# Kernel tuning notes

Measured on AMD Instinct MI355X. Metric: run time of the kernel, lower is better.

Reference implementation:

```python
import jax, jax.numpy as jnp
import numpy as np

NQ = 4  # n_qubits_per_head


def _apply_ry(state, theta, q):
    # state: (N, 2,2,2,2) real amplitudes; theta: (N,) per-element angle; wire q
    st = jnp.moveaxis(state, 1 + q, -1)
    c = jnp.cos(0.5 * theta).reshape(-1, 1, 1, 1)
    s = jnp.sin(0.5 * theta).reshape(-1, 1, 1, 1)
    a0, a1 = st[..., 0], st[..., 1]
    st = jnp.stack([c * a0 - s * a1, s * a0 + c * a1], axis=-1)
    return jnp.moveaxis(st, -1, 1 + q)


def _apply_cnot(state, ctrl, tgt):
    st = jnp.moveaxis(state, (1 + ctrl, 1 + tgt), (-2, -1))
    st = jnp.stack([st[..., 0, :], st[..., 1, ::-1]], axis=-2)
    return jnp.moveaxis(st, (-2, -1), (1 + ctrl, 1 + tgt))


def _quantum_circuit(x_in, par):
    # x_in: (N, NQ) data angles; par: (N, L, NQ) variational angles (per head, tiled)
    N = x_in.shape[0]
    L = par.shape[1]
    state = jnp.zeros((N, 2, 2, 2, 2), x_in.dtype).at[:, 0, 0, 0, 0].set(1.0)
    for l in range(L):
        for q in range(NQ):
            state = _apply_ry(state, par[:, l, q], q)
        for q in range(NQ - 1):
            state = _apply_cnot(state, q, q + 1)
        state = _apply_cnot(state, NQ - 1, 0)
    for q in range(NQ):
        state = _apply_ry(state, x_in[:, q], q)
    p = state * state  # probabilities (real amplitudes: only RY/CNOT gates)
    zs = []
    for q in range(NQ):
        st = jnp.moveaxis(p, 1 + q, -1)
        zs.append(jnp.sum(st[..., 0], axis=(1, 2, 3)) - jnp.sum(st[..., 1], axis=(1, 2, 3)))
    return jnp.stack(zs, axis=-1)  # (N, NQ)


def setup_inputs() -> dict:
    key = jax.random.key(0)
    ks = jax.random.split(key, 6)
    B, T, E, H, L = 4, 2048, 1024, 16, 2
    scale = 1.0 / np.sqrt(E)
    x = jax.random.normal(ks[0], (B, T, E), dtype=jnp.float32)
    Wq = jax.random.normal(ks[1], (E, E), dtype=jnp.float32) * scale
    Wk = jax.random.normal(ks[2], (E, E), dtype=jnp.float32) * scale
    Wv = jax.random.normal(ks[3], (E, E), dtype=jnp.float32) * scale
    Wo = jax.random.normal(ks[4], (E, E), dtype=jnp.float32) * scale
    qparams = jax.random.normal(ks[5], (H, L, NQ), dtype=jnp.float32)
    return {"x": x, "Wq": Wq, "Wk": Wk, "Wv": Wv, "Wo": Wo, "qparams": qparams}


def reference(x, Wq, Wk, Wv, Wo, qparams):
    B, T, E = x.shape
    H, L, _ = qparams.shape
    hd = E // H
    q = x @ Wq.T
    k = x @ Wk.T
    v = x @ Wv.T
    # NOTE: original scales by sqrt(embed_dim), not sqrt(head_dim)
    scores = jnp.einsum('bte,bse->bts', q, k) / jnp.sqrt(jnp.asarray(E, x.dtype))
    w = jax.nn.softmax(scores, axis=-1)
    out = jnp.einsum('bts,bse->bte', w, v)
    oh = out.reshape(B, T, H, hd)
    N = B * T * H
    xin = oh[..., :NQ].reshape(N, NQ)
    par = jnp.broadcast_to(qparams[None, None], (B, T, H, L, NQ)).reshape(N, L, NQ)
    z = _quantum_circuit(xin, par)  # (N, NQ)
    zfull = jnp.concatenate([z, jnp.zeros((N, hd - NQ), x.dtype)], axis=-1)
    return zfull.reshape(B, T, E) @ Wo.T
```

## Files before the change

kernel.cpp:

```cpp
#include <hip/hip_runtime.h>
#include <hip/hip_fp16.h>

typedef _Float16 half_t;
typedef __attribute__((ext_vector_type(8))) _Float16 half8;
typedef __attribute__((ext_vector_type(4))) float floatx4;

__device__ __forceinline__ void async_copy16(const void* src, void* dst_lds) {
  __builtin_amdgcn_global_load_lds(
      (__attribute__((address_space(1))) void*)src,
      (__attribute__((address_space(3))) void*)dst_lds, 16, 0, 0);
}

template<int BN, int EPI>
__global__ __launch_bounds__(256) void gemm_nt(
    const half_t* __restrict__ A, const half_t* __restrict__ B,
    void* __restrict__ Cout,
    int lda, int ldb, int ldc, int kIters, int zShift,
    long sAz1, long sBz1, long sCz1,
    long sAz2, long sBz2, long sCz2, float scale,
    const float* __restrict__ qab)
{
  constexpr int BM = 128;
  constexpr int WN = BN / 2;
  constexpr int AN = WN / 16;
  constexpr int RA = BM * 8 / 256;
  constexpr int RB = BN * 8 / 256;
  __shared__ __align__(16) half_t lA[BM * 64];
  __shared__ __align__(16) half_t lB[BN * 64];

  const int tid  = threadIdx.x;
  const int wave = tid >> 6, lane = tid & 63;
  const int wm = wave >> 1, wn = wave & 1;
  const int er = lane >> 4, ec = lane & 15;
  const int sw = ec & 7;

  const long z = blockIdx.z;
  const long z2 = z >> zShift;
  const long z1 = z - (z2 << zShift);
  const half_t* Ab = A + (long)blockIdx.x * BM * lda + z1 * sAz1 + z2 * sAz2;
  const half_t* Bb = B + (long)blockIdx.y * BN * ldb + z1 * sBz1 + z2 * sBz2;
  const long cz = z1 * sCz1 + z2 * sCz2;

  floatx4 acc[4][AN];
  #pragma unroll
  for (int i = 0; i < 4; i++)
    #pragma unroll
    for (int j = 0; j < AN; j++)
      acc[i][j] = (floatx4){0.f, 0.f, 0.f, 0.f};

  for (int ks = 0; ks < kIters; ++ks) {
    const half_t* Ak = Ab + ks * 64;
    const half_t* Bk = Bb + ks * 64;
    #pragma unroll
    for (int r = 0; r < RA; r++) {
      int s = r * 256 + tid;
      int row = s >> 3;
      int kq = (s & 7) ^ (row & 7);
      async_copy16(Ak + (long)row * lda + kq * 8,
                   &lA[(r * 256 + wave * 64) * 8]);
    }
    #pragma unroll
    for (int r = 0; r < RB; r++) {
      int s = r * 256 + tid;
      int row = s >> 3;
      int kq = (s & 7) ^ (row & 7);
      async_copy16(Bk + (long)row * ldb + kq * 8,
                   &lB[(r * 256 + wave * 64) * 8]);
    }
    __syncthreads();

    #pragma unroll
    for (int h = 0; h < 2; h++) {
      half8 af[4], bfv[AN];
      #pragma unroll
      for (int i = 0; i < 4; i++) {
        int row = wm * 64 + i * 16 + ec;
        af[i] = *(const half8*)&lA[row * 64 + (((h * 4 + er) ^ sw) * 8)];
      }
      #pragma unroll
      for (int j = 0; j < AN; j++) {
        int row = wn * WN + j * 16 + ec;
        bfv[j] = *(const half8*)&lB[row * 64 + (((h * 4 + er) ^ sw) * 8)];
      }
      #pragma unroll
      for (int i = 0; i < 4; i++)
        #pragma unroll
        for (int j = 0; j < AN; j++)
          acc[i][j] = __builtin_amdgcn_mfma_f32_16x16x32_f16(
              af[i], bfv[j], acc[i][j], 0, 0, 0);
    }
    __syncthreads();
  }

  const long rowBase = (long)blockIdx.x * BM + wm * 64;
  const long colBase = (long)blockIdx.y * BN + wn * WN;
  #pragma unroll
  for (int i = 0; i < 4; i++)
    #pragma unroll
    for (int j = 0; j < AN; j++)
      #pragma unroll
      for (int r = 0; r < 4; r++) {
        long row = rowBase + i * 16 + er * 4 + r;
        long col = colBase + j * 16 + ec;
        float v = acc[i][j][r];
        if constexpr (EPI == 0) {
          ((half_t*)Cout)[cz + row * (long)ldc + col] = (_Float16)(v * scale);
        } else if constexpr (EPI == 1) {
          ((half_t*)Cout)[cz + col * (long)ldc + row] = (_Float16)v;
        } else if constexpr (EPI == 2) {
          ((float*)Cout)[cz + row * (long)ldc + col] = v * scale;
        } else {
          float za = qab[2 * (int)col], zb = qab[2 * (int)col + 1];
          float zv = za * cosf(v) + zb * sinf(v);
          ((half_t*)Cout)[cz + row * (long)ldc + col] = (_Float16)zv;
        }
      }
}

__global__ __launch_bounds__(256) void softmax_rows(half_t* __restrict__ S,
                                                    int ld)
{
  const long row = blockIdx.x;
  half8* sp = (half8*)(S + row * (long)ld);
  const int t = threadIdx.x;
  const int wave = t >> 6, lane = t & 63;
  half8 hv = sp[t];
  float e[8];
  #pragma unroll
  for (int k = 0; k < 8; k++) e[k] = (float)hv[k];
  float m = e[0];
  #pragma unroll
  for (int k = 1; k < 8; k++) m = fmaxf(m, e[k]);
  #pragma unroll
  for (int o = 32; o > 0; o >>= 1) m = fmaxf(m, __shfl_xor(m, o));
  __shared__ float rmax[4], rsum[4];
  if (lane == 0) rmax[wave] = m;
  __syncthreads();
  m = fmaxf(fmaxf(rmax[0], rmax[1]), fmaxf(rmax[2], rmax[3]));
  float s = 0.f;
  #pragma unroll
  for (int k = 0; k < 8; k++) { e[k] = expf(e[k] - m); s += e[k]; }
  #pragma unroll
  for (int o = 32; o > 0; o >>= 1) s += __shfl_xor(s, o);
  if (lane == 0) rsum[wave] = s;
  __syncthreads();
  float inv = 1.f / (rsum[0] + rsum[1] + rsum[2] + rsum[3]);
  half8 o8;
  #pragma unroll
  for (int k = 0; k < 8; k++) o8[k] = (_Float16)(e[k] * inv);
  sp[t] = o8;
}

__global__ __launch_bounds__(256) void prep_all(
    const float* __restrict__ x,  const float* __restrict__ Wq,
    const float* __restrict__ Wk, const float* __restrict__ Wv,
    const float* __restrict__ Wo, const float* __restrict__ qp, int L,
    half_t* __restrict__ xh, half_t* __restrict__ Wqk,
    half_t* __restrict__ Wv4, half_t* __restrict__ Wos,
    float* __restrict__ qab)
{
  const int bid = blockIdx.x;
  if (bid < 4096) {
    long i = ((long)bid * 256 + threadIdx.x) * 8;
    float4 a = *(const float4*)(x + i);
    float4 b = *(const float4*)(x + i + 4);
    half8 h = {(_Float16)a.x, (_Float16)a.y, (_Float16)a.z, (_Float16)a.w,
               (_Float16)b.x, (_Float16)b.y, (_Float16)b.z, (_Float16)b.w};
    *(half8*)(xh + i) = h;
  } else if (bid < 5120) {
    long i = ((long)(bid - 4096) * 256 + threadIdx.x) * 8;
    int r = (int)(i >> 10);
    int e = (int)(i & 1023);
    const float* src = (r < 1024 ? Wq + (long)r * 1024
                                 : Wk + (long)(r - 1024) * 1024) + e;
    float4 a = *(const float4*)src;
    float4 b = *(const float4*)(src + 4);
    half8 h = {(_Float16)a.x, (_Float16)a.y, (_Float16)a.z, (_Float16)a.w,
               (_Float16)b.x, (_Float16)b.y, (_Float16)b.z, (_Float16)b.w};
    *(half8*)(Wqk + i) = h;
  } else if (bid < 5152) {
    long i = ((long)(bid - 5120) * 256 + threadIdx.x) * 8;
    int c = (int)(i >> 10);
    int e = (int)(i & 1023);
    const float* src = Wv + (long)(((c >> 2) << 6) | (c & 3)) * 1024 + e;
    float4 a = *(const float4*)src;
    float4 b = *(const float4*)(src + 4);
    half8 h = {(_Float16)a.x, (_Float16)a.y, (_Float16)a.z, (_Float16)a.w,
               (_Float16)b.x, (_Float16)b.y, (_Float16)b.z, (_Float16)b.w};
    *(half8*)(Wv4 + i) = h;
  } else if (bid < 5408) {
    int idx = (bid - 5152) * 256 + threadIdx.x;
    int e = idx >> 6, c = idx & 63;
    Wos[idx] = (_Float16)Wo[(long)e * 1024 + (((c >> 2) << 6) | (c & 3))];
  } else {
    int h = threadIdx.x;
    if (h >= 16) return;
    float st[16];
    #pragma unroll
    for (int i = 0; i < 16; i++) st[i] = 0.f;
    st[0] = 1.f;
    for (int l = 0; l < L; l++) {
      #pragma unroll
      for (int q = 0; q < 4; q++) {
        float th = qp[(h * L + l) * 4 + q];
        float c = cosf(0.5f * th), s = sinf(0.5f * th);
        int mq = 8 >> q;
        #pragma unroll
        for (int i = 0; i < 16; i++) {
          if ((i & mq) == 0) {
            float a0 = st[i], a1 = st[i | mq];
            st[i]      = c * a0 - s * a1;
            st[i | mq] = s * a0 + c * a1;
          }
        }
      }
      const int cm[4] = {8, 4, 2, 1};
      const int tm[4] = {4, 2, 1, 8};
      #pragma unroll
      for (int p = 0; p < 4; p++) {
        int mc = cm[p], mt = tm[p];
        #pragma unroll
        for (int i = 0; i < 16; i++) {
          if ((i & mc) != 0 && (i & mt) == 0) {
            float tv = st[i]; st[i] = st[i | mt]; st[i | mt] = tv;
          }
        }
      }
    }
    #pragma unroll
    for (int q = 0; q < 4; q++) {
      int mq = 8 >> q;
      float zc = 0.f, xc = 0.f;
      #pragma unroll
      for (int i = 0; i < 16; i++) {
        float p2 = st[i] * st[i];
        zc += ((i & mq) == 0) ? p2 : -p2;
        if ((i & mq) == 0) xc += st[i] * st[i | mq];
      }
      qab[(h * 4 + q) * 2 + 0] = zc;
      qab[(h * 4 + q) * 2 + 1] = -2.f * xc;
    }
  }
}

extern "C" void kernel_launch(void* const* d_in, const int* in_sizes, int n_in,
                              void* d_out, int out_size, void* d_ws, size_t ws_size,
                              hipStream_t stream)
{
  const float* x  = (const float*)d_in[0];
  const float* Wq = (const float*)d_in[1];
  const float* Wk = (const float*)d_in[2];
  const float* Wv = (const float*)d_in[3];
  const float* Wo = (const float*)d_in[4];
  const float* qp = (const float*)d_in[5];
  const int L = in_sizes[5] / 64;
  float* out = (float*)d_out;

  char* w = (char*)d_ws;
  size_t off = 0;
  auto alloc = [&](size_t bytes) -> void* {
    void* p = w + off;
    off = (off + bytes + 255) & ~(size_t)255;
    return p;
  };
  float*  qab  = (float*)alloc(512);
  half_t* xh   = (half_t*)alloc((size_t)8192 * 1024 * 2);
  half_t* Wqk  = (half_t*)alloc((size_t)2048 * 1024 * 2);
  half_t* Wv4  = (half_t*)alloc((size_t)64 * 1024 * 2);
  half_t* Wos  = (half_t*)alloc((size_t)1024 * 64 * 2);
  half_t* V4th = (half_t*)alloc((size_t)64 * 8192 * 2);
  half_t* Z4   = (half_t*)alloc((size_t)8192 * 64 * 2);

  half_t* QKb = (half_t*)d_out;

  int tier = (ws_size >= off + (size_t)8192 * 2048 * 2 + 256) ? 0 : 1;
  const size_t Sn = (tier == 0) ? (size_t)8192 * 2048 : (size_t)2048 * 2048;
  half_t* S = (half_t*)alloc(Sn * 2);

  prep_all<<<dim3(5409), dim3(256), 0, stream>>>(
      x, Wq, Wk, Wv, Wo, qp, L, xh, Wqk, Wv4, Wos, qab);

  gemm_nt<128, 0><<<dim3(64, 16, 1), 256, 0, stream>>>(
      xh, Wqk, QKb, 1024, 1024, 2048, 16, 0,
      0, 0, 0, 0, 0, 0, 1.f, nullptr);
  gemm_nt<64, 1><<<dim3(64, 1, 1), 256, 0, stream>>>(
      xh, Wv4, V4th, 1024, 1024, 8192, 16, 0,
      0, 0, 0, 0, 0, 0, 1.f, nullptr);

  if (tier == 0) {
    gemm_nt<128, 0><<<dim3(16, 16, 4), 256, 0, stream>>>(
        QKb, QKb + 1024, S, 2048, 2048, 2048, 16, 0,
        0, 0, 0, (long)2048 * 2048, (long)2048 * 2048, (long)2048 * 2048,
        0.03125f, nullptr);
    softmax_rows<<<dim3(8192), dim3(256), 0, stream>>>(S, 2048);
    gemm_nt<64, 5><<<dim3(16, 1, 4), 256, 0, stream>>>(
        S, V4th, Z4, 2048, 8192, 64, 32, 0,
        0, 0, 0, (long)2048 * 2048, 2048, (long)2048 * 64, 1.f, qab);
  } else {
    for (int b = 0; b < 4; b++) {
      const long q0 = (long)b * 2048;
      gemm_nt<128, 0><<<dim3(16, 16, 1), 256, 0, stream>>>(
          QKb + q0 * 2048, QKb + 1024 + q0 * 2048, S,
          2048, 2048, 2048, 16, 0, 0, 0, 0, 0, 0, 0, 0.03125f, nullptr);
      softmax_rows<<<dim3(2048), dim3(256), 0, stream>>>(S, 2048);
      gemm_nt<64, 5><<<dim3(16, 1, 1), 256, 0, stream>>>(
          S, V4th + q0, Z4 + q0 * 64, 2048, 8192, 64, 32, 0,
          0, 0, 0, 0, 0, 0, 1.f, qab);
    }
  }

  gemm_nt<128, 2><<<dim3(64, 8, 1), 256, 0, stream>>>(
      Z4, Wos, out, 64, 64, 1024, 1, 0, 0, 0, 0, 0, 0, 0, 1.f, nullptr);
}
```

Baseline: 263.1 us.

## Fold Wq and Wk into one matrix and fuse V projection into single GEMM

Scores are now computed as x·(Wq^T Wk)·x^T. A small 1024x1024 GEMM precomputes Wq^T·Wk, and a combined GEMM produces y = x·M together with the four V columns per head, so separate Q and K projections are no longer needed. Writing S into the output buffer also removes the workspace-size tier and always runs the batched path. The cost is the extra weight-product GEMM and strided transposing writes in prep. Rounding the folded matrix to fp16 changes precision slightly.

Result: slower. 271.1 us (+3.0%).

```diff
diff --git a/kernel.cpp b/kernel.cpp
--- a/kernel.cpp
+++ b/kernel.cpp
@@ -18,7 +18,7 @@
     int lda, int ldb, int ldc, int kIters, int zShift,
     long sAz1, long sBz1, long sCz1,
     long sAz2, long sBz2, long sCz2, float scale,
-    const float* __restrict__ qab)
+    const void* __restrict__ aux)
 {
   constexpr int BM = 128;
   constexpr int WN = BN / 2;
@@ -105,14 +105,19 @@
         float v = acc[i][j][r];
         if constexpr (EPI == 0) {
           ((half_t*)Cout)[cz + row * (long)ldc + col] = (_Float16)(v * scale);
-        } else if constexpr (EPI == 1) {
-          ((half_t*)Cout)[cz + col * (long)ldc + row] = (_Float16)v;
         } else if constexpr (EPI == 2) {
           ((float*)Cout)[cz + row * (long)ldc + col] = v * scale;
-        } else {
+        } else if constexpr (EPI == 5) {
+          const float* qab = (const float*)aux;
           float za = qab[2 * (int)col], zb = qab[2 * (int)col + 1];
           float zv = za * cosf(v) + zb * sinf(v);
           ((half_t*)Cout)[cz + row * (long)ldc + col] = (_Float16)zv;
+        } else {
+          if (col < 1024) {
+            ((half_t*)Cout)[row * 1024 + col] = (_Float16)v;
+          } else if (col < 1088) {
+            ((half_t*)aux)[(col - 1024) * 8192 + row] = (_Float16)v;
+          }
         }
       }
 }
@@ -155,9 +160,9 @@
     const float* __restrict__ x,  const float* __restrict__ Wq,
     const float* __restrict__ Wk, const float* __restrict__ Wv,
     const float* __restrict__ Wo, const float* __restrict__ qp, int L,
-    half_t* __restrict__ xh, half_t* __restrict__ Wqk,
-    half_t* __restrict__ Wv4, half_t* __restrict__ Wos,
-    float* __restrict__ qab)
+    half_t* __restrict__ xh, half_t* __restrict__ WqT,
+    half_t* __restrict__ WkT, half_t* __restrict__ Wcat,
+    half_t* __restrict__ Wos, float* __restrict__ qab)
 {
   const int bid = blockIdx.x;
   if (bid < 4096) {
@@ -168,16 +173,17 @@
                (_Float16)b.x, (_Float16)b.y, (_Float16)b.z, (_Float16)b.w};
     *(half8*)(xh + i) = h;
   } else if (bid < 5120) {
-    long i = ((long)(bid - 4096) * 256 + threadIdx.x) * 8;
-    int r = (int)(i >> 10);
-    int e = (int)(i & 1023);
-    const float* src = (r < 1024 ? Wq + (long)r * 1024
-                                 : Wk + (long)(r - 1024) * 1024) + e;
-    float4 a = *(const float4*)src;
-    float4 b = *(const float4*)(src + 4);
-    half8 h = {(_Float16)a.x, (_Float16)a.y, (_Float16)a.z, (_Float16)a.w,
-               (_Float16)b.x, (_Float16)b.y, (_Float16)b.z, (_Float16)b.w};
-    *(half8*)(Wqk + i) = h;
+    const int base = bid < 4608 ? 4096 : 4608;
+    const float* src = bid < 4608 ? Wq : Wk;
+    half_t* dst = bid < 4608 ? WqT : WkT;
+    long i = ((long)(bid - base) * 256 + threadIdx.x) * 8;
+    int r = (int)(i >> 10), c = (int)(i & 1023);
+    float4 a = *(const float4*)(src + (long)r * 1024 + c);
+    float4 b = *(const float4*)(src + (long)r * 1024 + c + 4);
+    float vv[8] = {a.x, a.y, a.z, a.w, b.x, b.y, b.z, b.w};
+    #pragma unroll
+    for (int j = 0; j < 8; j++)
+      dst[(long)(c + j) * 1024 + r] = (_Float16)vv[j];
   } else if (bid < 5152) {
     long i = ((long)(bid - 5120) * 256 + threadIdx.x) * 8;
     int c = (int)(i >> 10);
@@ -187,9 +193,12 @@
     float4 b = *(const float4*)(src + 4);
     half8 h = {(_Float16)a.x, (_Float16)a.y, (_Float16)a.z, (_Float16)a.w,
                (_Float16)b.x, (_Float16)b.y, (_Float16)b.z, (_Float16)b.w};
-    *(half8*)(Wv4 + i) = h;
-  } else if (bid < 5408) {
-    int idx = (bid - 5152) * 256 + threadIdx.x;
+    *(half8*)(Wcat + (long)1024 * 1024 + i) = h;
+  } else if (bid < 5184) {
+    long i = ((long)(bid - 5152) * 256 + threadIdx.x) * 8;
+    *(half8*)(Wcat + (long)1088 * 1024 + i) = (half8){0,0,0,0,0,0,0,0};
+  } else if (bid < 5440) {
+    int idx = (bid - 5184) * 256 + threadIdx.x;
     int e = idx >> 6, c = idx & 63;
     Wos[idx] = (_Float16)Wo[(long)e * 1024 + (((c >> 2) << 6) | (c & 3))];
   } else {
@@ -265,49 +274,37 @@
   };
   float*  qab  = (float*)alloc(512);
   half_t* xh   = (half_t*)alloc((size_t)8192 * 1024 * 2);
-  half_t* Wqk  = (half_t*)alloc((size_t)2048 * 1024 * 2);
-  half_t* Wv4  = (half_t*)alloc((size_t)64 * 1024 * 2);
+  half_t* WqT  = (half_t*)alloc((size_t)1024 * 1024 * 2);
+  half_t* WkT  = (half_t*)alloc((size_t)1024 * 1024 * 2);
+  half_t* Wcat = (half_t*)alloc((size_t)1152 * 1024 * 2);
   half_t* Wos  = (half_t*)alloc((size_t)1024 * 64 * 2);
   half_t* V4th = (half_t*)alloc((size_t)64 * 8192 * 2);
+  half_t* y    = (half_t*)alloc((size_t)8192 * 1024 * 2);
   half_t* Z4   = (half_t*)alloc((size_t)8192 * 64 * 2);
 
-  half_t* QKb = (half_t*)d_out;
-
-  int tier = (ws_size >= off + (size_t)8192 * 2048 * 2 + 256) ? 0 : 1;
-  const size_t Sn = (tier == 0) ? (size_t)8192 * 2048 : (size_t)2048 * 2048;
-  half_t* S = (half_t*)alloc(Sn * 2);
-
-  prep_all<<<dim3(5409), dim3(256), 0, stream>>>(
-      x, Wq, Wk, Wv, Wo, qp, L, xh, Wqk, Wv4, Wos, qab);
-
-  gemm_nt<128, 0><<<dim3(64, 16, 1), 256, 0, stream>>>(
-      xh, Wqk, QKb, 1024, 1024, 2048, 16, 0,
+  half_t* S = (half_t*)d_out;
+
+  prep_all<<<dim3(5441), dim3(256), 0, stream>>>(
+      x, Wq, Wk, Wv, Wo, qp, L, xh, WqT, WkT, Wcat, Wos, qab);
+
+  gemm_nt<64, 0><<<dim3(8, 16, 1), 256, 0, stream>>>(
+      WkT, WqT, Wcat, 1024, 1024, 1024, 16, 0,
       0, 0, 0, 0, 0, 0, 1.f, nullptr);
-  gemm_nt<64, 1><<<dim3(64, 1, 1), 256, 0, stream>>>(
-      xh, Wv4, V4th, 1024, 1024, 8192, 16, 0,
-      0, 0, 0, 0, 0, 0, 1.f, nullptr);
-
-  if (tier == 0) {
-    gemm_nt<128, 0><<<dim3(16, 16, 4), 256, 0, stream>>>(
-        QKb, QKb + 1024, S, 2048, 2048, 2048, 16, 0,
-        0, 0, 0, (long)2048 * 2048, (long)2048 * 2048, (long)2048 * 2048,
-        0.03125f, nullptr);
-    softmax_rows<<<dim3(8192), dim3(256), 0, stream>>>(S, 2048);
-    gemm_nt<64, 5><<<dim3(16, 1, 4), 256, 0, stream>>>(
-        S, V4th, Z4, 2048, 8192, 64, 32, 0,
-        0, 0, 0, (long)2048 * 2048, 2048, (long)2048 * 64, 1.f, qab);
-  } else {
-    for (int b = 0; b < 4; b++) {
-      const long q0 = (long)b * 2048;
-      gemm_nt<128, 0><<<dim3(16, 16, 1), 256, 0, stream>>>(
-          QKb + q0 * 2048, QKb + 1024 + q0 * 2048, S,
-          2048, 2048, 2048, 16, 0, 0, 0, 0, 0, 0, 0, 0.03125f, nullptr);
-      softmax_rows<<<dim3(2048), dim3(256), 0, stream>>>(S, 2048);
-      gemm_nt<64, 5><<<dim3(16, 1, 1), 256, 0, stream>>>(
-          S, V4th + q0, Z4 + q0 * 64, 2048, 8192, 64, 32, 0,
-          0, 0, 0, 0, 0, 0, 1.f, qab);
-    }
-  }
+
+  gemm_nt<128, 6><<<dim3(64, 9, 1), 256, 0, stream>>>(
+      xh, Wcat, y, 1024, 1024, 1024, 16, 0,
+      0, 0, 0, 0, 0, 0, 1.f, V4th);
+
+  gemm_nt<128, 0><<<dim3(16, 16, 4), 256, 0, stream>>>(
+      y, xh, S, 1024, 1024, 2048, 16, 0,
+      0, 0, 0, (long)2048 * 1024, (long)2048 * 1024, (long)2048 * 2048,
+      0.03125f, nullptr);
+
+  softmax_rows<<<dim3(8192), dim3(256), 0, stream>>>(S, 2048);
+
+  gemm_nt<64, 5><<<dim3(16, 1, 4), 256, 0, stream>>>(
+      S, V4th, Z4, 2048, 8192, 64, 32, 0,
+      0, 0, 0, (long)2048 * 2048, 2048, (long)2048 * 64, 1.f, qab);
 
   gemm_nt<128, 2><<<dim3(64, 8, 1), 256, 0, stream>>>(
       Z4, Wos, out, 64, 64, 1024, 1, 0, 0, 0, 0, 0, 0, 0, 1.f, nullptr);
```
